# Optimization experiments

Measured on AMD Instinct MI355X. Metric: run time of the kernel, lower is better.

## Reference

```python
import jax, jax.numpy as jnp
import numpy as np

D_MODEL = 1024
N_HEADS = 16
D_K = D_MODEL // N_HEADS


def setup_inputs() -> dict:
    key = jax.random.key(0)
    ks = jax.random.split(key, 9)
    s = 1.0 / np.sqrt(D_MODEL)
    def lin(kw, kb):
        W = jax.random.uniform(kw, (D_MODEL, D_MODEL), jnp.float32, -s, s)
        b = jax.random.uniform(kb, (D_MODEL,), jnp.float32, -s, s)
        return W, b
    wq, bq = lin(ks[0], ks[1])
    wk, bk = lin(ks[2], ks[3])
    wv, bv = lin(ks[4], ks[5])
    wo, bo = lin(ks[6], ks[7])
    x = jax.random.normal(ks[8], (2, 2048, D_MODEL), jnp.float32)
    return {"x": x, "wq": wq, "bq": bq, "wk": wk, "bk": bk,
            "wv": wv, "bv": bv, "wo": wo, "bo": bo}


def reference(x, wq, bq, wk, bk, wv, bv, wo, bo):
    B, S, D = x.shape
    scale = 1.0 / np.sqrt(D_K)
    # projections (torch Linear: y = x W^T + b); W stored as [in,out] here
    q = x @ wq + bq
    k = x @ wk + bk
    v = x @ wv + bv
    # [B, H, S, d_k]
    q = q.reshape(B, S, N_HEADS, D_K).transpose(0, 2, 1, 3)
    k = k.reshape(B, S, N_HEADS, D_K).transpose(0, 2, 1, 3)
    v = v.reshape(B, S, N_HEADS, D_K).transpose(0, 2, 1, 3)
    scores = jnp.einsum('bhqd,bhkd->bhqk', q, k) * scale
    attn = jax.nn.softmax(scores, axis=-1)
    out = jnp.einsum('bhqk,bhkd->bhqd', attn, v)
    out = out.transpose(0, 2, 1, 3).reshape(B, S, D)
    return out @ wo + bo
```

## Files before the change

### kernel.cpp

```cpp
#include <hip/hip_runtime.h>
#include <hip/hip_bf16.h>
#include <math.h>

typedef __bf16 bf16x8 __attribute__((ext_vector_type(8)));
typedef unsigned short u16x8 __attribute__((ext_vector_type(8)));
typedef unsigned short u16x4 __attribute__((ext_vector_type(4)));
typedef float f32x4 __attribute__((ext_vector_type(4)));
typedef unsigned short u16;

__device__ __forceinline__ u16 f2bf(float f) {
    unsigned int x = __float_as_uint(f);
    x += 0x7fffu + ((x >> 16) & 1u);
    return (u16)(x >> 16);
}
__device__ __forceinline__ void glds16(const void* g, void* l) {
    __builtin_amdgcn_global_load_lds(
        (const __attribute__((address_space(1))) void*)g,
        (__attribute__((address_space(3))) void*)l, 16, 0, 0);
}

__global__ __launch_bounds__(256) void prep(const float* __restrict__ W0, const float* __restrict__ W1,
                                            const float* __restrict__ W2, const float* __restrict__ W3,
                                            const float* __restrict__ X,
                                            u16* __restrict__ Wt, u16* __restrict__ Xb) {
    int z = blockIdx.z;
    if (z >= 4) {
        int row = (z - 4) * 1024 + blockIdx.y * 32 + blockIdx.x;
        const float* src = X + (size_t)row * 1024 + threadIdx.x * 4;
        f32x4 v = *(const f32x4*)src;
        u16x4 o; o[0] = f2bf(v[0]); o[1] = f2bf(v[1]); o[2] = f2bf(v[2]); o[3] = f2bf(v[3]);
        *(u16x4*)&Xb[(size_t)row * 1024 + threadIdx.x * 4] = o;
        return;
    }
    __shared__ float T[32][33];
    const float* W = (z == 0) ? W0 : ((z == 1) ? W1 : ((z == 2) ? W2 : W3));
    u16* dst = Wt + (size_t)z * 1024 * 1024;
    int k0 = blockIdx.y * 32, n0 = blockIdx.x * 32;
    int x = threadIdx.x & 31, y0 = threadIdx.x >> 5;
#pragma unroll
    for (int i = 0; i < 4; i++) {
        int y = y0 + i * 8;
        T[y][x] = W[(size_t)(k0 + y) * 1024 + n0 + x];
    }
    __syncthreads();
#pragma unroll
    for (int i = 0; i < 4; i++) {
        int y = y0 + i * 8;
        dst[(size_t)(n0 + y) * 1024 + k0 + x] = f2bf(T[x][y]);
    }
}

template <bool OF32, bool VSPLIT>
__global__ __launch_bounds__(256) void gemm(
    const u16* __restrict__ Bt,
    const float* __restrict__ b0, const float* __restrict__ b1, const float* __restrict__ b2,
    const u16* __restrict__ A, void* __restrict__ Cptr, u16* __restrict__ Vt, int Ntot)
{
    __shared__ __align__(16) u16 As[128 * 32];
    __shared__ __align__(16) u16 Bs[128 * 32];
    int tid = threadIdx.x;
    int lane = tid & 63, l15 = lane & 15, quad = lane >> 4;
    int wid = tid >> 6, wm = wid >> 1, wn = wid & 1;
    int m0 = blockIdx.y * 128, n0 = blockIdx.x * 128;
    int sel = n0 >> 10;
    const float* bias = (sel == 0) ? b0 : ((sel == 1) ? b1 : b2);

    f32x4 acc[4][4];
#pragma unroll
    for (int i = 0; i < 4; i++)
#pragma unroll
        for (int j = 0; j < 4; j++) { f32x4 z = {0.f, 0.f, 0.f, 0.f}; acc[i][j] = z; }

    int rr = lane >> 2;
    int cc = (lane & 3) ^ ((rr >> 1) & 3);
    const u16* abase = A  + (size_t)m0 * 1024;
    const u16* bbase = Bt + (size_t)n0 * 1024;
    int fsw = (l15 >> 1) & 3;

    for (int k0 = 0; k0 < 1024; k0 += 32) {
#pragma unroll
        for (int inst = 0; inst < 2; inst++) {
            int r0 = wid * 32 + inst * 16;
            glds16(&abase[(size_t)(r0 + rr) * 1024 + k0 + cc * 8], &As[r0 * 32]);
            glds16(&bbase[(size_t)(r0 + rr) * 1024 + k0 + cc * 8], &Bs[r0 * 32]);
        }
        __syncthreads();
        bf16x8 af[4], bf[4];
#pragma unroll
        for (int mt = 0; mt < 4; mt++)
            af[mt] = *(const bf16x8*)&As[(wm * 64 + mt * 16 + l15) * 32 + ((quad ^ fsw) * 8)];
#pragma unroll
        for (int nt = 0; nt < 4; nt++)
            bf[nt] = *(const bf16x8*)&Bs[(wn * 64 + nt * 16 + l15) * 32 + ((quad ^ fsw) * 8)];
#pragma unroll
        for (int mt = 0; mt < 4; mt++)
#pragma unroll
            for (int nt = 0; nt < 4; nt++)
                acc[mt][nt] = __builtin_amdgcn_mfma_f32_16x16x32_bf16(af[mt], bf[nt], acc[mt][nt], 0, 0, 0);
        __syncthreads();
    }
    if (VSPLIT && sel == 2) {
        int b = m0 >> 11;
#pragma unroll
        for (int mt = 0; mt < 4; mt++) {
            int gr = m0 + wm * 64 + mt * 16 + quad * 4;
            int s = gr & 2047;
#pragma unroll
            for (int nt = 0; nt < 4; nt++) {
                int gcl = (n0 & 1023) + wn * 64 + nt * 16 + l15;
                float bb = bias[gcl];
                u16x4 pk;
#pragma unroll
                for (int r = 0; r < 4; r++) pk[r] = f2bf(acc[mt][nt][r] + bb);
                *(u16x4*)&Vt[(size_t)((b * 16 + (gcl >> 6)) * 64 + (gcl & 63)) * 2048 + s] = pk;
            }
        }
        return;
    }
#pragma unroll
    for (int mt = 0; mt < 4; mt++) {
        int gr = m0 + wm * 64 + mt * 16 + quad * 4;
#pragma unroll
        for (int nt = 0; nt < 4; nt++) {
            int gc = n0 + wn * 64 + nt * 16 + l15;
            float bb = bias[gc & 1023];
#pragma unroll
            for (int r = 0; r < 4; r++) {
                float v = acc[mt][nt][r] + bb;
                if (OF32) ((float*)Cptr)[(size_t)(gr + r) * Ntot + gc] = v;
                else      ((u16*)Cptr)[(size_t)(gr + r) * Ntot + gc] = f2bf(v);
            }
        }
    }
}

__global__ __launch_bounds__(256) void attn(const u16* __restrict__ QKV,
                                            const u16* __restrict__ Vt,
                                            u16* __restrict__ O)
{
    __shared__ __align__(16) u16 Ks[64 * 64];
    __shared__ __align__(16) u16 Vs[64 * 64];
    __shared__ __align__(16) u16 Ps[4][16 * 72];
    const int S = 2048, DQ = 3072;
    int tid = threadIdx.x, wid = tid >> 6, lane = tid & 63;
    int l15 = lane & 15, quad = lane >> 4;
    int qt = blockIdx.x, h = blockIdx.y, b = blockIdx.z;
    const u16* base = QKV + (size_t)b * S * DQ + h * 64;
    const u16* Kb = base + 1024;
    const u16* Vtb = Vt + (size_t)((b * 16 + h) * 64) * 2048;
    int q0 = qt * 64 + wid * 16;

    bf16x8 qf0 = *(const bf16x8*)&base[(size_t)(q0 + l15) * DQ + quad * 8];
    bf16x8 qf1 = *(const bf16x8*)&base[(size_t)(q0 + l15) * DQ + 32 + quad * 8];

    f32x4 oacc[4];
#pragma unroll
    for (int i = 0; i < 4; i++) { f32x4 z = {0.f, 0.f, 0.f, 0.f}; oacc[i] = z; }
    float psum[4] = {0.f, 0.f, 0.f, 0.f};
    const float ls = 0.125f * 1.44269504088896f;

    int rr = lane >> 3;
    int cc = (lane & 7) ^ rr;
    int fs7 = l15 & 7;

    for (int kv0 = 0; kv0 < S; kv0 += 64) {
#pragma unroll
        for (int inst = 0; inst < 2; inst++) {
            int r0 = wid * 16 + inst * 8;
            glds16(&Kb[(size_t)(kv0 + r0 + rr) * DQ + cc * 8], &Ks[r0 * 64]);
            glds16(&Vtb[(size_t)(r0 + rr) * 2048 + kv0 + cc * 8], &Vs[r0 * 64]);
        }
        __syncthreads();

        f32x4 sa[4];
#pragma unroll
        for (int t = 0; t < 4; t++) { f32x4 z = {0.f, 0.f, 0.f, 0.f}; sa[t] = z; }
#pragma unroll
        for (int t = 0; t < 4; t++) {
            bf16x8 kfa = *(const bf16x8*)&Ks[(t * 16 + l15) * 64 + ((quad ^ fs7) * 8)];
            bf16x8 kfb = *(const bf16x8*)&Ks[(t * 16 + l15) * 64 + (((quad + 4) ^ fs7) * 8)];
            sa[t] = __builtin_amdgcn_mfma_f32_16x16x32_bf16(qf0, kfa, sa[t], 0, 0, 0);
            sa[t] = __builtin_amdgcn_mfma_f32_16x16x32_bf16(qf1, kfb, sa[t], 0, 0, 0);
        }
        u16* Pw = Ps[wid];
#pragma unroll
        for (int t = 0; t < 4; t++)
#pragma unroll
            for (int r = 0; r < 4; r++) {
                float p = __builtin_amdgcn_exp2f(sa[t][r] * ls);
                psum[r] += p;
                Pw[(quad * 4 + r) * 72 + t * 16 + l15] = f2bf(p);
            }
        __asm__ __volatile__("" ::: "memory");
        bf16x8 pf0 = *(const bf16x8*)&Pw[l15 * 72 + quad * 8];
        bf16x8 pf1 = *(const bf16x8*)&Pw[l15 * 72 + 32 + quad * 8];
#pragma unroll
        for (int dt = 0; dt < 4; dt++) {
            bf16x8 vfa = *(const bf16x8*)&Vs[(dt * 16 + l15) * 64 + ((quad ^ fs7) * 8)];
            bf16x8 vfb = *(const bf16x8*)&Vs[(dt * 16 + l15) * 64 + (((quad + 4) ^ fs7) * 8)];
            oacc[dt] = __builtin_amdgcn_mfma_f32_16x16x32_bf16(pf0, vfa, oacc[dt], 0, 0, 0);
            oacc[dt] = __builtin_amdgcn_mfma_f32_16x16x32_bf16(pf1, vfb, oacc[dt], 0, 0, 0);
        }
        __syncthreads();
    }
#pragma unroll
    for (int r = 0; r < 4; r++) {
        float s = psum[r];
        s += __shfl_xor(s, 1);
        s += __shfl_xor(s, 2);
        s += __shfl_xor(s, 4);
        s += __shfl_xor(s, 8);
        float inv = 1.0f / s;
        size_t row = (size_t)(b * S + q0 + quad * 4 + r);
#pragma unroll
        for (int dt = 0; dt < 4; dt++)
            O[row * 1024 + h * 64 + dt * 16 + l15] = f2bf(oacc[dt][r] * inv);
    }
}

extern "C" void kernel_launch(void* const* d_in, const int* in_sizes, int n_in,
                              void* d_out, int out_size, void* d_ws, size_t ws_size,
                              hipStream_t stream) {
    const float* x  = (const float*)d_in[0];
    const float* wq = (const float*)d_in[1];
    const float* bq = (const float*)d_in[2];
    const float* wk = (const float*)d_in[3];
    const float* bk = (const float*)d_in[4];
    const float* wv = (const float*)d_in[5];
    const float* bv = (const float*)d_in[6];
    const float* wo = (const float*)d_in[7];
    const float* bo = (const float*)d_in[8];
    float* out = (float*)d_out;

    u16* qkv  = (u16*)d_ws;
    u16* obuf = qkv  + (size_t)4096 * 3072;
    u16* vt   = obuf + (size_t)4096 * 1024;
    u16* wt   = vt   + (size_t)2048 * 2048;
    u16* xb   = wt   + (size_t)4 * 1024 * 1024;

    dim3 tb(256);
    prep<<<dim3(32, 32, 8), tb, 0, stream>>>(wq, wk, wv, wo, x, wt, xb);
    gemm<false, true><<<dim3(24, 32), tb, 0, stream>>>(wt, bq, bk, bv, xb, qkv, vt, 3072);
    attn<<<dim3(32, 16, 2), tb, 0, stream>>>(qkv, vt, obuf);
    gemm<true, false><<<dim3(8, 32), tb, 0, stream>>>(wt + (size_t)3 * 1024 * 1024,
                                                      bo, bo, bo, obuf, out, (u16*)nullptr, 1024);
}
```

Baseline: 220.5 us.

## Double-buffer K/V tiles and keep P in registers via transposed QK^T and permlane swaps

```diff
diff --git a/kernel.cpp b/kernel.cpp
--- a/kernel.cpp
+++ b/kernel.cpp
@@ -6,6 +6,8 @@
 typedef unsigned short u16x8 __attribute__((ext_vector_type(8)));
 typedef unsigned short u16x4 __attribute__((ext_vector_type(4)));
 typedef float f32x4 __attribute__((ext_vector_type(4)));
+typedef unsigned int u32x4 __attribute__((ext_vector_type(4)));
+typedef unsigned int u32x2 __attribute__((ext_vector_type(2)));
 typedef unsigned short u16;
 
 __device__ __forceinline__ u16 f2bf(float f) {
@@ -17,6 +19,11 @@
     __builtin_amdgcn_global_load_lds(
         (const __attribute__((address_space(1))) void*)g,
         (__attribute__((address_space(3))) void*)l, 16, 0, 0);
+}
+__device__ __forceinline__ void swap_half(unsigned& a, unsigned& b) {
+    u32x2 t = __builtin_amdgcn_permlane32_swap(a, b, false, false);
+    t = __builtin_amdgcn_permlane16_swap(t[0], t[1], false, false);
+    a = t[0]; b = t[1];
 }
 
 __global__ __launch_bounds__(256) void prep(const float* __restrict__ W0, const float* __restrict__ W1,
@@ -138,9 +145,8 @@
                                             const u16* __restrict__ Vt,
                                             u16* __restrict__ O)
 {
-    __shared__ __align__(16) u16 Ks[64 * 64];
-    __shared__ __align__(16) u16 Vs[64 * 64];
-    __shared__ __align__(16) u16 Ps[4][16 * 72];
+    __shared__ __align__(16) u16 Ks[2][64 * 64];
+    __shared__ __align__(16) u16 Vs[2][64 * 64];
     const int S = 2048, DQ = 3072;
     int tid = threadIdx.x, wid = tid >> 6, lane = tid & 63;
     int l15 = lane & 15, quad = lane >> 4;
@@ -156,61 +162,80 @@
     f32x4 oacc[4];
 #pragma unroll
     for (int i = 0; i < 4; i++) { f32x4 z = {0.f, 0.f, 0.f, 0.f}; oacc[i] = z; }
-    float psum[4] = {0.f, 0.f, 0.f, 0.f};
+    float psum = 0.f;
     const float ls = 0.125f * 1.44269504088896f;
 
     int rr = lane >> 3;
     int cc = (lane & 7) ^ rr;
     int fs7 = l15 & 7;
 
-    for (int kv0 = 0; kv0 < S; kv0 += 64) {
+    auto stage = [&](int it, int bsel) {
+        int kv0 = it << 6;
 #pragma unroll
         for (int inst = 0; inst < 2; inst++) {
             int r0 = wid * 16 + inst * 8;
-            glds16(&Kb[(size_t)(kv0 + r0 + rr) * DQ + cc * 8], &Ks[r0 * 64]);
-            glds16(&Vtb[(size_t)(r0 + rr) * 2048 + kv0 + cc * 8], &Vs[r0 * 64]);
-        }
-        __syncthreads();
+            glds16(&Kb[(size_t)(kv0 + r0 + rr) * DQ + cc * 8], &Ks[bsel][r0 * 64]);
+            glds16(&Vtb[(size_t)(r0 + rr) * 2048 + kv0 + cc * 8], &Vs[bsel][r0 * 64]);
+        }
+    };
+
+    stage(0, 0);
+#pragma unroll 2
+    for (int it = 0; it < 32; ++it) {
+        int cur = it & 1;
+        if (it < 31) {
+            stage(it + 1, cur ^ 1);
+            asm volatile("s_waitcnt vmcnt(4)\n\ts_barrier" ::: "memory");
+        } else {
+            asm volatile("s_waitcnt vmcnt(0)\n\ts_barrier" ::: "memory");
+        }
 
         f32x4 sa[4];
 #pragma unroll
         for (int t = 0; t < 4; t++) { f32x4 z = {0.f, 0.f, 0.f, 0.f}; sa[t] = z; }
 #pragma unroll
         for (int t = 0; t < 4; t++) {
-            bf16x8 kfa = *(const bf16x8*)&Ks[(t * 16 + l15) * 64 + ((quad ^ fs7) * 8)];
-            bf16x8 kfb = *(const bf16x8*)&Ks[(t * 16 + l15) * 64 + (((quad + 4) ^ fs7) * 8)];
-            sa[t] = __builtin_amdgcn_mfma_f32_16x16x32_bf16(qf0, kfa, sa[t], 0, 0, 0);
-            sa[t] = __builtin_amdgcn_mfma_f32_16x16x32_bf16(qf1, kfb, sa[t], 0, 0, 0);
-        }
-        u16* Pw = Ps[wid];
-#pragma unroll
-        for (int t = 0; t < 4; t++)
-#pragma unroll
-            for (int r = 0; r < 4; r++) {
-                float p = __builtin_amdgcn_exp2f(sa[t][r] * ls);
-                psum[r] += p;
-                Pw[(quad * 4 + r) * 72 + t * 16 + l15] = f2bf(p);
-            }
-        __asm__ __volatile__("" ::: "memory");
-        bf16x8 pf0 = *(const bf16x8*)&Pw[l15 * 72 + quad * 8];
-        bf16x8 pf1 = *(const bf16x8*)&Pw[l15 * 72 + 32 + quad * 8];
+            bf16x8 kfa = *(const bf16x8*)&Ks[cur][(t * 16 + l15) * 64 + ((quad ^ fs7) * 8)];
+            bf16x8 kfb = *(const bf16x8*)&Ks[cur][(t * 16 + l15) * 64 + (((quad + 4) ^ fs7) * 8)];
+            sa[t] = __builtin_amdgcn_mfma_f32_16x16x32_bf16(kfa, qf0, sa[t], 0, 0, 0);
+            sa[t] = __builtin_amdgcn_mfma_f32_16x16x32_bf16(kfb, qf1, sa[t], 0, 0, 0);
+        }
+
+        unsigned wpk[4][2];
+#pragma unroll
+        for (int t = 0; t < 4; t++) {
+            float e0 = __builtin_amdgcn_exp2f(sa[t][0] * ls);
+            float e1 = __builtin_amdgcn_exp2f(sa[t][1] * ls);
+            float e2 = __builtin_amdgcn_exp2f(sa[t][2] * ls);
+            float e3 = __builtin_amdgcn_exp2f(sa[t][3] * ls);
+            psum += (e0 + e1) + (e2 + e3);
+            asm("v_cvt_pk_bf16_f32 %0, %1, %2" : "=v"(wpk[t][0]) : "v"(e0), "v"(e1));
+            asm("v_cvt_pk_bf16_f32 %0, %1, %2" : "=v"(wpk[t][1]) : "v"(e2), "v"(e3));
+        }
+        unsigned a0 = wpk[0][0], a2 = wpk[1][0]; swap_half(a0, a2);
+        unsigned a1 = wpk[0][1], a3 = wpk[1][1]; swap_half(a1, a3);
+        unsigned c0 = wpk[2][0], c2 = wpk[3][0]; swap_half(c0, c2);
+        unsigned c1 = wpk[2][1], c3 = wpk[3][1]; swap_half(c1, c3);
+        u32x4 pd0 = {a0, a1, a2, a3};
+        u32x4 pd1 = {c0, c1, c2, c3};
+        bf16x8 pf0 = *(bf16x8*)&pd0;
+        bf16x8 pf1 = *(bf16x8*)&pd1;
+
 #pragma unroll
         for (int dt = 0; dt < 4; dt++) {
-            bf16x8 vfa = *(const bf16x8*)&Vs[(dt * 16 + l15) * 64 + ((quad ^ fs7) * 8)];
-            bf16x8 vfb = *(const bf16x8*)&Vs[(dt * 16 + l15) * 64 + (((quad + 4) ^ fs7) * 8)];
+            bf16x8 vfa = *(const bf16x8*)&Vs[cur][(dt * 16 + l15) * 64 + ((quad ^ fs7) * 8)];
+            bf16x8 vfb = *(const bf16x8*)&Vs[cur][(dt * 16 + l15) * 64 + (((quad + 4) ^ fs7) * 8)];
             oacc[dt] = __builtin_amdgcn_mfma_f32_16x16x32_bf16(pf0, vfa, oacc[dt], 0, 0, 0);
             oacc[dt] = __builtin_amdgcn_mfma_f32_16x16x32_bf16(pf1, vfb, oacc[dt], 0, 0, 0);
         }
-        __syncthreads();
-    }
+        asm volatile("s_barrier" ::: "memory");
+    }
+
+    psum += __shfl_xor(psum, 16);
+    psum += __shfl_xor(psum, 32);
 #pragma unroll
     for (int r = 0; r < 4; r++) {
-        float s = psum[r];
-        s += __shfl_xor(s, 1);
-        s += __shfl_xor(s, 2);
-        s += __shfl_xor(s, 4);
-        s += __shfl_xor(s, 8);
-        float inv = 1.0f / s;
+        float inv = 1.0f / __shfl(psum, quad * 4 + r);
         size_t row = (size_t)(b * S + q0 + quad * 4 + r);
 #pragma unroll
         for (int dt = 0; dt < 4; dt++)
```

New measurement: 210.1 us. 1.05x faster.
